# Kernel tuning notes

Hardware: AMD Instinct MI355X
Metric: run time of the kernel (lower is better)

## Reference

```python
import jax, jax.numpy as jnp
import numpy as np

MAX_EMBED = 1024
MAX_HEADS = 16
MIN_WIDTH_RATIO = 0.25


def setup_inputs() -> dict:
    key = jax.random.key(0)
    ks = jax.random.split(key, 10)
    B, S, E = 4, 1024, MAX_EMBED
    query = jax.random.normal(ks[0], (B, S, E), dtype=jnp.float32)
    attention_mask = jax.random.randint(ks[1], (B, 1, 1, S), 0, 2, dtype=jnp.int32)
    # SlimmableLinear params (max sizes); kaiming-ish scale ~ 1/sqrt(fan_in)
    scale = 1.0 / np.sqrt(E)
    def lin(kw, kb):
        w = jax.random.uniform(kw, (E, E), dtype=jnp.float32, minval=-scale, maxval=scale)
        b = jax.random.uniform(kb, (E,), dtype=jnp.float32, minval=-scale, maxval=scale)
        return w, b
    q_w, q_b = lin(ks[2], ks[3])
    k_w, k_b = lin(ks[4], ks[5])
    v_w, v_b = lin(ks[6], ks[7])
    o_w, o_b = lin(ks[8], ks[9])
    return {"query": query, "attention_mask": attention_mask,
            "q_w": q_w, "q_b": q_b, "k_w": k_w, "k_b": k_b,
            "v_w": v_w, "v_b": v_b, "o_w": o_w, "o_b": o_b,
            "width": 768}


def _slim_linear(x, w, b, width):
    # weight stored [out, in] like torch; slice to [width, width]
    return x[..., :width] @ w[:width, :width].T + b[:width]


def reference(query, attention_mask, q_w, q_b, k_w, k_b, v_w, v_b, o_w, o_b, width):
    min_width = int(MAX_EMBED * MIN_WIDTH_RATIO)
    width = max(min_width, min(int(width), MAX_EMBED))
    num_heads = max(1, width * MAX_HEADS // MAX_EMBED)
    head_dim = width // num_heads
    B, S, _ = query.shape

    q = _slim_linear(query, q_w, q_b, width)  # [B,S,width]
    k = _slim_linear(query, k_w, k_b, width)  # key=query (self-attn)
    v = _slim_linear(query, v_w, v_b, width)

    q = q.reshape(B, S, num_heads, head_dim).transpose(0, 2, 1, 3)  # [B,H,S,D]
    k = k.reshape(B, S, num_heads, head_dim).transpose(0, 2, 1, 3)
    v = v.reshape(B, S, num_heads, head_dim).transpose(0, 2, 1, 3)

    scores = jnp.einsum('bhqd,bhkd->bhqk', q, k) / jnp.sqrt(jnp.float32(head_dim))
    scores = jnp.where(attention_mask == 0, jnp.float32(-1e9), scores)
    attn_weights = jax.nn.softmax(scores, axis=-1)  # [B,H,S,S]
    attn_output = jnp.einsum('bhqk,bhkd->bhqd', attn_weights, v)
    attn_output = attn_output.transpose(0, 2, 1, 3).reshape(B, S, width)
    output = attn_output @ o_w[:width, :width].T + o_b[:width]
    return output, attn_weights
```

## Files before the change

### kernel.cpp

```cpp
#include <hip/hip_runtime.h>

#define Bn 4
#define Sn 1024
#define En 1024
#define Wn 768
#define Hn 12
#define Dn 64
#define XE ((size_t)Bn * Sn * Wn)

typedef __attribute__((ext_vector_type(8))) short short8;
typedef __attribute__((ext_vector_type(4))) short short4v;
typedef __attribute__((ext_vector_type(4))) float floatx4;

#define MFMA16(A, B, C) __builtin_amdgcn_mfma_f32_16x16x32_bf16(A, B, C, 0, 0, 0)

__device__ __forceinline__ unsigned short f2bf_rn(float f) {
    unsigned int u = __float_as_uint(f);
    unsigned int r = u + 0x7fffu + ((u >> 16) & 1u);
    return (unsigned short)(r >> 16);
}
__device__ __forceinline__ float bf2f(unsigned short h) {
    return __uint_as_float(((unsigned int)h) << 16);
}

__device__ __forceinline__ void gload_lds16(const unsigned short* g, unsigned short* l) {
    __builtin_amdgcn_global_load_lds(
        (const __attribute__((address_space(1))) void*)g,
        (__attribute__((address_space(3))) void*)l, 16, 0, 0);
}

__global__ __launch_bounds__(256) void prep_kernel(
    const float* __restrict__ x,
    const float* __restrict__ qw, const float* __restrict__ kw,
    const float* __restrict__ vw, const float* __restrict__ ow,
    const float* __restrict__ qb, const float* __restrict__ kb,
    const float* __restrict__ vb,
    unsigned short* __restrict__ xh, unsigned short* __restrict__ xl,
    unsigned short* __restrict__ wqh, unsigned short* __restrict__ wql,
    unsigned short* __restrict__ woh, unsigned short* __restrict__ wol,
    float* __restrict__ bq)
{
    const int bx = blockIdx.x;
    const float* src; unsigned short *dh, *dl; int e;
    if (bx < 3072) {
        e = (bx * 256 + threadIdx.x) * 4;
        src = x; dh = xh; dl = xl;
    } else if (bx < 3072 + 1728) {
        int bb = bx - 3072; int which = bb / 576;
        e = ((bb - which * 576) * 256 + threadIdx.x) * 4;
        src = (which == 0) ? qw : (which == 1) ? kw : vw;
        dh = wqh + (size_t)which * Wn * Wn;
        dl = wql + (size_t)which * Wn * Wn;
    } else if (bx < 3072 + 1728 + 576) {
        e = ((bx - 3072 - 1728) * 256 + threadIdx.x) * 4;
        src = ow; dh = woh; dl = wol;
    } else {
        int t = (bx - 3072 - 1728 - 576) * 256 + threadIdx.x;
        if (t < Wn) bq[t] = qb[t];
        else if (t < 2 * Wn) bq[t] = kb[t - Wn];
        else if (t < 3 * Wn) bq[t] = vb[t - 2 * Wn];
        return;
    }
    int row = e / Wn, col = e - row * Wn;
    float4 v = *(const float4*)(src + (size_t)row * En + col);
    float f[4] = {v.x, v.y, v.z, v.w};
    short4v h, l;
    #pragma unroll
    for (int i = 0; i < 4; ++i) {
        unsigned short hh = f2bf_rn(f[i]);
        h[i] = (short)hh;
        l[i] = (short)f2bf_rn(f[i] - bf2f(hh));
    }
    *(short4v*)(dh + e) = h;
    *(short4v*)(dl + e) = l;
}

__global__ __launch_bounds__(256) void qkv_mfma_kernel(
    const unsigned short* __restrict__ xh, const unsigned short* __restrict__ xl,
    const unsigned short* __restrict__ wh, const unsigned short* __restrict__ wl,
    const float* __restrict__ bq,
    float* __restrict__ q32, float* __restrict__ k32,
    unsigned short* __restrict__ vt_o)
{
    __shared__ __align__(16) unsigned short Ah[128 * 32];
    __shared__ __align__(16) unsigned short Al[128 * 32];
    __shared__ __align__(16) unsigned short Bh[128 * 32];
    __shared__ __align__(16) unsigned short Bl[128 * 32];

    const int tid = threadIdx.x;
    const int wave = tid >> 6, lane = tid & 63;
    const int quad = lane >> 4, l16 = lane & 15;
    const int m0 = blockIdx.x * 128, n0 = blockIdx.y * 128;
    const int wm = wave >> 1, wn = wave & 1;

    floatx4 acc[4][4] = {};

    const unsigned short* gsrc = (wave == 0) ? xh : (wave == 1) ? xl
                               : (wave == 2) ? wh : wl;
    unsigned short* ldst = (wave == 0) ? Ah : (wave == 1) ? Al
                         : (wave == 2) ? Bh : Bl;
    const int base_row = (wave < 2) ? m0 : n0;
    const int r_in = lane >> 2;
    const int cs = (lane & 3) ^ (r_in & 3);

    for (int k0 = 0; k0 < Wn; k0 += 32) {
        #pragma unroll
        for (int i = 0; i < 8; ++i) {
            int r = i * 16 + r_in;
            const unsigned short* gp =
                gsrc + (size_t)(base_row + r) * Wn + k0 + cs * 8;
            gload_lds16(gp, ldst + i * 512);
        }
        __syncthreads();

        short8 afh[4], afl[4], bfh[4], bfl[4];
        #pragma unroll
        for (int t = 0; t < 4; ++t) {
            int mr = wm * 64 + t * 16 + l16;
            int ca = quad ^ (mr & 3);
            afh[t] = *(const short8*)(Ah + mr * 32 + ca * 8);
            afl[t] = *(const short8*)(Al + mr * 32 + ca * 8);
            int nr = wn * 64 + t * 16 + l16;
            int cb = quad ^ (nr & 3);
            bfh[t] = *(const short8*)(Bh + nr * 32 + cb * 8);
            bfl[t] = *(const short8*)(Bl + nr * 32 + cb * 8);
        }
        #pragma unroll
        for (int mt = 0; mt < 4; ++mt)
            #pragma unroll
            for (int nt = 0; nt < 4; ++nt) {
                acc[mt][nt] = MFMA16(afh[mt], bfh[nt], acc[mt][nt]);
                acc[mt][nt] = MFMA16(afh[mt], bfl[nt], acc[mt][nt]);
                acc[mt][nt] = MFMA16(afl[mt], bfh[nt], acc[mt][nt]);
            }
        __syncthreads();
    }

    const int which = n0 / Wn;
    const int b = m0 >> 10;
    #pragma unroll
    for (int nt = 0; nt < 4; ++nt) {
        const int ng = n0 + wn * 64 + nt * 16 + l16;
        const float bias = bq[ng];
        const int f = ng - which * Wn;
        const int h = f >> 6, d = f & 63;
        #pragma unroll
        for (int mt = 0; mt < 4; ++mt) {
            const int mbase = m0 + wm * 64 + mt * 16 + quad * 4;
            const int s0 = mbase & (Sn - 1);
            if (which < 2) {
                float* o32 = which ? k32 : q32;
                size_t idx = (((size_t)(b * Hn + h)) * Sn + s0) * Dn + d;
                #pragma unroll
                for (int r = 0; r < 4; ++r)
                    o32[idx + (size_t)r * Dn] = acc[mt][nt][r] + bias;
            } else {
                size_t idx = (((size_t)(b * Hn + h)) * Dn + d) * Sn + s0;
                short4v pk;
                #pragma unroll
                for (int r = 0; r < 4; ++r)
                    pk[r] = (short)f2bf_rn(acc[mt][nt][r] + bias);
                *(short4v*)(vt_o + idx) = pk;
            }
        }
    }
}

__global__ __launch_bounds__(256) void attn_sum_kernel(
    const float* __restrict__ q32, const float* __restrict__ k32,
    const int* __restrict__ mask, float* __restrict__ lpart)
{
    __shared__ __align__(16) unsigned short Kh[64 * 72];
    __shared__ __align__(16) unsigned short Kl[64 * 72];
    __shared__ float msk[64];

    const int tid = threadIdx.x;
    const int wave = tid >> 6, lane = tid & 63;
    const int quad = lane >> 4, l16 = lane & 15;
    const int qt = blockIdx.x >> 2, ks = blockIdx.x & 3;
    const int h = blockIdx.y, b = blockIdx.z;
    const int bh = b * Hn + h;
    const size_t kvb = (size_t)bh * Sn * Dn;

    short8 qfh[2], qfl[2];
    {
        const int s = qt * 64 + wave * 16 + l16;
        const float* qp = q32 + kvb + (size_t)s * Dn + quad * 8;
        #pragma unroll
        for (int ksp = 0; ksp < 2; ++ksp) {
            float f[8];
            *(float4*)&f[0] = *(const float4*)(qp + ksp * 32);
            *(float4*)&f[4] = *(const float4*)(qp + ksp * 32 + 4);
            #pragma unroll
            for (int j = 0; j < 8; ++j) {
                unsigned short hh = f2bf_rn(f[j]);
                qfh[ksp][j] = (short)hh;
                qfl[ksp][j] = (short)f2bf_rn(f[j] - bf2f(hh));
            }
        }
    }

    const int sr = tid >> 2, sc = tid & 3;
    float lsum[4] = {0.f, 0.f, 0.f, 0.f};

    for (int kt = 0; kt < 4; ++kt) {
        __syncthreads();
        {
            const float* kp = k32 + kvb + (size_t)(ks * 256 + kt * 64 + sr) * Dn + sc * 16;
            float f[16];
            *(float4*)&f[0]  = *(const float4*)(kp);
            *(float4*)&f[4]  = *(const float4*)(kp + 4);
            *(float4*)&f[8]  = *(const float4*)(kp + 8);
            *(float4*)&f[12] = *(const float4*)(kp + 12);
            short8 h0, h1, l0, l1;
            #pragma unroll
            for (int j = 0; j < 8; ++j) {
                unsigned short hh = f2bf_rn(f[j]);
                h0[j] = (short)hh; l0[j] = (short)f2bf_rn(f[j] - bf2f(hh));
                unsigned short hh2 = f2bf_rn(f[8 + j]);
                h1[j] = (short)hh2; l1[j] = (short)f2bf_rn(f[8 + j] - bf2f(hh2));
            }
            *(short8*)&Kh[sr * 72 + sc * 16]     = h0;
            *(short8*)&Kh[sr * 72 + sc * 16 + 8] = h1;
            *(short8*)&Kl[sr * 72 + sc * 16]     = l0;
            *(short8*)&Kl[sr * 72 + sc * 16 + 8] = l1;
            if (tid < 64) msk[tid] = (float)mask[b * Sn + ks * 256 + kt * 64 + tid];
        }
        __syncthreads();
        #pragma unroll
        for (int ct = 0; ct < 4; ++ct) {
            floatx4 acc = {0.f, 0.f, 0.f, 0.f};
            const int key = ct * 16 + l16;
            #pragma unroll
            for (int ksp = 0; ksp < 2; ++ksp) {
                short8 b8h = *(const short8*)&Kh[key * 72 + ksp * 32 + quad * 8];
                short8 b8l = *(const short8*)&Kl[key * 72 + ksp * 32 + quad * 8];
                acc = MFMA16(qfh[ksp], b8h, acc);
                acc = MFMA16(qfh[ksp], b8l, acc);
                acc = MFMA16(qfl[ksp], b8h, acc);
            }
            const float mv = msk[key];
            #pragma unroll
            for (int r = 0; r < 4; ++r)
                lsum[r] += __expf(acc[r] * 0.125f) * mv;
        }
    }

    #pragma unroll
    for (int r = 0; r < 4; ++r) {
        float v = lsum[r];
        v += __shfl_xor(v, 1, 64);
        v += __shfl_xor(v, 2, 64);
        v += __shfl_xor(v, 4, 64);
        v += __shfl_xor(v, 8, 64);
        lsum[r] = v;
    }
    if (l16 == 0) {
        const int row = qt * 64 + wave * 16 + quad * 4;
        #pragma unroll
        for (int r = 0; r < 4; ++r)
            lpart[((size_t)ks * Bn * Hn + bh) * Sn + row + r] = lsum[r];
    }
}

__global__ __launch_bounds__(256) void attn_out_kernel(
    const float* __restrict__ q32, const float* __restrict__ k32,
    const unsigned short* __restrict__ vt, const int* __restrict__ mask,
    const float* __restrict__ lpart, float* __restrict__ attn,
    float* __restrict__ opart)
{
    __shared__ __align__(16) unsigned short Kh[64 * 72];
    __shared__ __align__(16) unsigned short Kl[64 * 72];
    __shared__ __align__(16) unsigned short Vs[64 * 72];
    __shared__ __align__(16) unsigned short Ps[4][16 * 72];
    __shared__ float msk[64];

    const int tid = threadIdx.x;
    const int wave = tid >> 6, lane = tid & 63;
    const int quad = lane >> 4, l16 = lane & 15;
    const int qt = blockIdx.x >> 2, ks = blockIdx.x & 3;
    const int h = blockIdx.y, b = blockIdx.z;
    const int bh = b * Hn + h;
    const size_t kvb = (size_t)bh * Sn * Dn;

    short8 qfh[2], qfl[2];
    {
        const int s = qt * 64 + wave * 16 + l16;
        const float* qp = q32 + kvb + (size_t)s * Dn + quad * 8;
        #pragma unroll
        for (int ksp = 0; ksp < 2; ++ksp) {
            float f[8];
            *(float4*)&f[0] = *(const float4*)(qp + ksp * 32);
            *(float4*)&f[4] = *(const float4*)(qp + ksp * 32 + 4);
            #pragma unroll
            for (int j = 0; j < 8; ++j) {
                unsigned short hh = f2bf_rn(f[j]);
                qfh[ksp][j] = (short)hh;
                qfl[ksp][j] = (short)f2bf_rn(f[j] - bf2f(hh));
            }
        }
    }

    float li[4];
    {
        const int row = qt * 64 + wave * 16 + quad * 4;
        #pragma unroll
        for (int r = 0; r < 4; ++r) {
            float lv = 0.f;
            #pragma unroll
            for (int s4 = 0; s4 < 4; ++s4)
                lv += lpart[((size_t)s4 * Bn * Hn + bh) * Sn + row + r];
            li[r] = (lv > 0.f) ? 1.f / lv : 0.f;
        }
    }

    const int sr = tid >> 2, sc = tid & 3;
    const size_t vbase = (size_t)bh * Dn * Sn;
    floatx4 oacc[4] = {};

    for (int kt = 0; kt < 4; ++kt) {
        __syncthreads();
        {
            const float* kp = k32 + kvb + (size_t)(ks * 256 + kt * 64 + sr) * Dn + sc * 16;
            float f[16];
            *(float4*)&f[0]  = *(const float4*)(kp);
            *(float4*)&f[4]  = *(const float4*)(kp + 4);
            *(float4*)&f[8]  = *(const float4*)(kp + 8);
            *(float4*)&f[12] = *(const float4*)(kp + 12);
            short8 h0, h1, l0, l1;
            #pragma unroll
            for (int j = 0; j < 8; ++j) {
                unsigned short hh = f2bf_rn(f[j]);
                h0[j] = (short)hh; l0[j] = (short)f2bf_rn(f[j] - bf2f(hh));
                unsigned short hh2 = f2bf_rn(f[8 + j]);
                h1[j] = (short)hh2; l1[j] = (short)f2bf_rn(f[8 + j] - bf2f(hh2));
            }
            *(short8*)&Kh[sr * 72 + sc * 16]     = h0;
            *(short8*)&Kh[sr * 72 + sc * 16 + 8] = h1;
            *(short8*)&Kl[sr * 72 + sc * 16]     = l0;
            *(short8*)&Kl[sr * 72 + sc * 16 + 8] = l1;
            const size_t g2 = vbase + (size_t)sr * Sn + ks * 256 + kt * 64 + sc * 16;
            *(short8*)&Vs[sr * 72 + sc * 16]     = *(const short8*)(vt + g2);
            *(short8*)&Vs[sr * 72 + sc * 16 + 8] = *(const short8*)(vt + g2 + 8);
            if (tid < 64) msk[tid] = (float)mask[b * Sn + ks * 256 + kt * 64 + tid];
        }
        __syncthreads();

        #pragma unroll
        for (int ct = 0; ct < 4; ++ct) {
            floatx4 acc = {0.f, 0.f, 0.f, 0.f};
            const int key = ct * 16 + l16;
            #pragma unroll
            for (int ksp = 0; ksp < 2; ++ksp) {
                short8 b8h = *(const short8*)&Kh[key * 72 + ksp * 32 + quad * 8];
                short8 b8l = *(const short8*)&Kl[key * 72 + ksp * 32 + quad * 8];
                acc = MFMA16(qfh[ksp], b8h, acc);
                acc = MFMA16(qfh[ksp], b8l, acc);
                acc = MFMA16(qfl[ksp], b8h, acc);
            }
            const float mv = msk[key];
            const int row0 = qt * 64 + wave * 16 + quad * 4;
            const int key_g = ks * 256 + kt * 64 + key;
            #pragma unroll
            for (int r = 0; r < 4; ++r) {
                float p = __expf(acc[r] * 0.125f) * mv * li[r];
                attn[((size_t)bh * Sn + row0 + r) * Sn + key_g] = p;
                Ps[wave][(quad * 4 + r) * 72 + key] = f2bf_rn(p);
            }
        }
        #pragma unroll
        for (int ksp = 0; ksp < 2; ++ksp) {
            short8 pf = *(const short8*)&Ps[wave][l16 * 72 + ksp * 32 + quad * 8];
            #pragma unroll
            for (int dt = 0; dt < 4; ++dt) {
                short8 vf = *(const short8*)&Vs[(dt * 16 + l16) * 72 + ksp * 32 + quad * 8];
                oacc[dt] = MFMA16(pf, vf, oacc[dt]);
            }
        }
    }

    const int s0 = qt * 64 + wave * 16 + quad * 4;
    #pragma unroll
    for (int dt = 0; dt < 4; ++dt)
        #pragma unroll
        for (int r = 0; r < 4; ++r)
            opart[(size_t)ks * XE + ((size_t)b * Sn + s0 + r) * Wn
                  + h * Dn + dt * 16 + l16] = oacc[dt][r];
}

__global__ __launch_bounds__(256) void reduce_ao_kernel(
    const float* __restrict__ opart, unsigned short* __restrict__ aoh,
    unsigned short* __restrict__ aol)
{
    size_t e = ((size_t)blockIdx.x * 256 + threadIdx.x) * 4;
    float4 a0 = *(const float4*)(opart + e);
    float4 a1 = *(const float4*)(opart + XE + e);
    float4 a2 = *(const float4*)(opart + 2 * XE + e);
    float4 a3 = *(const float4*)(opart + 3 * XE + e);
    float f[4] = {a0.x + a1.x + a2.x + a3.x, a0.y + a1.y + a2.y + a3.y,
                  a0.z + a1.z + a2.z + a3.z, a0.w + a1.w + a2.w + a3.w};
    short4v h, l;
    #pragma unroll
    for (int i = 0; i < 4; ++i) {
        unsigned short hh = f2bf_rn(f[i]);
        h[i] = (short)hh;
        l[i] = (short)f2bf_rn(f[i] - bf2f(hh));
    }
    *(short4v*)(aoh + e) = h;
    *(short4v*)(aol + e) = l;
}

__global__ __launch_bounds__(256) void oproj_mfma_kernel(
    const unsigned short* __restrict__ aoh, const unsigned short* __restrict__ aol,
    const unsigned short* __restrict__ wh, const unsigned short* __restrict__ wl,
    const float* __restrict__ ob, float* __restrict__ out)
{
    __shared__ __align__(16) unsigned short Ah[64 * 32];
    __shared__ __align__(16) unsigned short Al[64 * 32];
    __shared__ __align__(16) unsigned short Bh[128 * 32];
    __shared__ __align__(16) unsigned short Bl[128 * 32];

    const int tid = threadIdx.x;
    const int wave = tid >> 6, lane = tid & 63;
    const int quad = lane >> 4, l16 = lane & 15;
    const int m0 = blockIdx.x * 64, n0 = blockIdx.y * 128;
    const int wm = wave >> 1, wn = wave & 1;

    floatx4 acc[2][4] = {};

    const int r_in = lane >> 2;
    const int cs = (lane & 3) ^ (r_in & 3);

    for (int k0 = 0; k0 < Wn; k0 += 32) {
        if (wave == 0) {
            #pragma unroll
            for (int i = 0; i < 4; ++i) {
                gload_lds16(aoh + (size_t)(m0 + i * 16 + r_in) * Wn + k0 + cs * 8,
                            Ah + i * 512);
                gload_lds16(aol + (size_t)(m0 + i * 16 + r_in) * Wn + k0 + cs * 8,
                            Al + i * 512);
            }
        } else if (wave == 1) {
            #pragma unroll
            for (int i = 0; i < 8; ++i)
                gload_lds16(wh + (size_t)(n0 + i * 16 + r_in) * Wn + k0 + cs * 8,
                            Bh + i * 512);
        } else if (wave == 2) {
            #pragma unroll
            for (int i = 0; i < 8; ++i)
                gload_lds16(wl + (size_t)(n0 + i * 16 + r_in) * Wn + k0 + cs * 8,
                            Bl + i * 512);
        }
        __syncthreads();

        short8 afh[2], afl[2], bfh[4], bfl[4];
        #pragma unroll
        for (int t = 0; t < 2; ++t) {
            int mr = wm * 32 + t * 16 + l16;
            int ca = quad ^ (mr & 3);
            afh[t] = *(const short8*)(Ah + mr * 32 + ca * 8);
            afl[t] = *(const short8*)(Al + mr * 32 + ca * 8);
        }
        #pragma unroll
        for (int t = 0; t < 4; ++t) {
            int nr = wn * 64 + t * 16 + l16;
            int cb = quad ^ (nr & 3);
            bfh[t] = *(const short8*)(Bh + nr * 32 + cb * 8);
            bfl[t] = *(const short8*)(Bl + nr * 32 + cb * 8);
        }
        #pragma unroll
        for (int mt = 0; mt < 2; ++mt)
            #pragma unroll
            for (int nt = 0; nt < 4; ++nt) {
                acc[mt][nt] = MFMA16(afh[mt], bfh[nt], acc[mt][nt]);
                acc[mt][nt] = MFMA16(afh[mt], bfl[nt], acc[mt][nt]);
                acc[mt][nt] = MFMA16(afl[mt], bfh[nt], acc[mt][nt]);
            }
        __syncthreads();
    }

    #pragma unroll
    for (int nt = 0; nt < 4; ++nt) {
        const int ng = n0 + wn * 64 + nt * 16 + l16;
        const float bias = ob[ng];
        #pragma unroll
        for (int mt = 0; mt < 2; ++mt) {
            const int m = m0 + wm * 32 + mt * 16 + quad * 4;
            #pragma unroll
            for (int r = 0; r < 4; ++r)
                out[(size_t)(m + r) * Wn + ng] = acc[mt][nt][r] + bias;
        }
    }
}

extern "C" void kernel_launch(void* const* d_in, const int* in_sizes, int n_in,
                              void* d_out, int out_size, void* d_ws, size_t ws_size,
                              hipStream_t stream) {
    const float* x    = (const float*)d_in[0];
    const int*   mask = (const int*)  d_in[1];
    const float* qw = (const float*)d_in[2];
    const float* qb = (const float*)d_in[3];
    const float* kw = (const float*)d_in[4];
    const float* kb = (const float*)d_in[5];
    const float* vw = (const float*)d_in[6];
    const float* vb = (const float*)d_in[7];
    const float* ow = (const float*)d_in[8];
    const float* ob = (const float*)d_in[9];

    float* out  = (float*)d_out;
    float* attn = out + XE;

    char* w = (char*)d_ws;
    unsigned short* xh   = (unsigned short*)w;  w += XE * 2;
    unsigned short* xl   = (unsigned short*)w;  w += XE * 2;
    unsigned short* wqh  = (unsigned short*)w;  w += (size_t)3 * Wn * Wn * 2;
    unsigned short* wql  = (unsigned short*)w;  w += (size_t)3 * Wn * Wn * 2;
    unsigned short* woh  = (unsigned short*)w;  w += (size_t)Wn * Wn * 2;
    unsigned short* wol  = (unsigned short*)w;  w += (size_t)Wn * Wn * 2;
    float*          bq   = (float*)w;           w += (size_t)3 * Wn * 4;
    float*          q32  = (float*)w;           w += XE * 4;
    float*          k32  = (float*)w;           w += XE * 4;
    unsigned short* vt_w = (unsigned short*)w;  w += XE * 2;
    float*          lpart = (float*)w;          w += (size_t)4 * Bn * Hn * Sn * 4;
    float*          opart = (float*)w;          w += (size_t)4 * XE * 4;

    prep_kernel<<<5385, 256, 0, stream>>>(x, qw, kw, vw, ow, qb, kb, vb,
                                          xh, xl, wqh, wql, woh, wol, bq);

    qkv_mfma_kernel<<<dim3(32, 18), 256, 0, stream>>>(
        xh, xl, wqh, wql, bq, q32, k32, vt_w);

    attn_sum_kernel<<<dim3(64, Hn, Bn), 256, 0, stream>>>(
        q32, k32, mask, lpart);

    attn_out_kernel<<<dim3(64, Hn, Bn), 256, 0, stream>>>(
        q32, k32, vt_w, mask, lpart, attn, opart);

    reduce_ao_kernel<<<3072, 256, 0, stream>>>(opart, xh, xl);

    oproj_mfma_kernel<<<dim3(64, 6), 256, 0, stream>>>(
        xh, xl, woh, wol, ob, out);
}
```

Baseline: 443.6 us.

## Use single bf16 Q/K, read K/V directly, and fuse the split-key reduction into attn_out

The QKV projection now stores Q and K as single bf16 values, and drops the low-part A term for those outputs. Both attention kernels then run one MFMA pass per score instead of three split-precision passes, and read K and V fragments straight from global memory instead of staging them in LDS. attn_out now walks all keys per block, so the 4-way key-split partial outputs and the separate reduce kernel go away, and it writes the hi/lo bf16 attention output directly. This cuts conversion work, MFMA count, syncs and partial-buffer traffic. The cost is lower precision in the scores and attention weights, which may break accuracy tolerances, plus fewer blocks and uncached global fragment loads in attn_out.

```diff
diff --git a/kernel.cpp b/kernel.cpp
--- a/kernel.cpp
+++ b/kernel.cpp
@@ -79,7 +79,7 @@
     const unsigned short* __restrict__ xh, const unsigned short* __restrict__ xl,
     const unsigned short* __restrict__ wh, const unsigned short* __restrict__ wl,
     const float* __restrict__ bq,
-    float* __restrict__ q32, float* __restrict__ k32,
+    unsigned short* __restrict__ qh_o, unsigned short* __restrict__ kh_o,
     unsigned short* __restrict__ vt_o)
 {
     __shared__ __align__(16) unsigned short Ah[128 * 32];
@@ -92,6 +92,8 @@
     const int quad = lane >> 4, l16 = lane & 15;
     const int m0 = blockIdx.x * 128, n0 = blockIdx.y * 128;
     const int wm = wave >> 1, wn = wave & 1;
+    const int which = n0 / Wn;
+    const bool full = (which == 2);
 
     floatx4 acc[4][4] = {};
 
@@ -104,12 +106,14 @@
     const int cs = (lane & 3) ^ (r_in & 3);
 
     for (int k0 = 0; k0 < Wn; k0 += 32) {
-        #pragma unroll
-        for (int i = 0; i < 8; ++i) {
-            int r = i * 16 + r_in;
-            const unsigned short* gp =
-                gsrc + (size_t)(base_row + r) * Wn + k0 + cs * 8;
-            gload_lds16(gp, ldst + i * 512);
+        if (full || wave != 1) {
+            #pragma unroll
+            for (int i = 0; i < 8; ++i) {
+                int r = i * 16 + r_in;
+                const unsigned short* gp =
+                    gsrc + (size_t)(base_row + r) * Wn + k0 + cs * 8;
+                gload_lds16(gp, ldst + i * 512);
+            }
         }
         __syncthreads();
 
@@ -119,7 +123,7 @@
             int mr = wm * 64 + t * 16 + l16;
             int ca = quad ^ (mr & 3);
             afh[t] = *(const short8*)(Ah + mr * 32 + ca * 8);
-            afl[t] = *(const short8*)(Al + mr * 32 + ca * 8);
+            if (full) afl[t] = *(const short8*)(Al + mr * 32 + ca * 8);
             int nr = wn * 64 + t * 16 + l16;
             int cb = quad ^ (nr & 3);
             bfh[t] = *(const short8*)(Bh + nr * 32 + cb * 8);
@@ -131,12 +135,11 @@
             for (int nt = 0; nt < 4; ++nt) {
                 acc[mt][nt] = MFMA16(afh[mt], bfh[nt], acc[mt][nt]);
                 acc[mt][nt] = MFMA16(afh[mt], bfl[nt], acc[mt][nt]);
-                acc[mt][nt] = MFMA16(afl[mt], bfh[nt], acc[mt][nt]);
+                if (full) acc[mt][nt] = MFMA16(afl[mt], bfh[nt], acc[mt][nt]);
             }
         __syncthreads();
     }
 
-    const int which = n0 / Wn;
     const int b = m0 >> 10;
     #pragma unroll
     for (int nt = 0; nt < 4; ++nt) {
@@ -149,11 +152,11 @@
             const int mbase = m0 + wm * 64 + mt * 16 + quad * 4;
             const int s0 = mbase & (Sn - 1);
             if (which < 2) {
-                float* o32 = which ? k32 : q32;
+                unsigned short* oq = which ? kh_o : qh_o;
                 size_t idx = (((size_t)(b * Hn + h)) * Sn + s0) * Dn + d;
                 #pragma unroll
                 for (int r = 0; r < 4; ++r)
-                    o32[idx + (size_t)r * Dn] = acc[mt][nt][r] + bias;
+                    oq[idx + (size_t)r * Dn] = f2bf_rn(acc[mt][nt][r] + bias);
             } else {
                 size_t idx = (((size_t)(b * Hn + h)) * Dn + d) * Sn + s0;
                 short4v pk;
@@ -167,13 +170,9 @@
 }
 
 __global__ __launch_bounds__(256) void attn_sum_kernel(
-    const float* __restrict__ q32, const float* __restrict__ k32,
+    const unsigned short* __restrict__ qh, const unsigned short* __restrict__ kh,
     const int* __restrict__ mask, float* __restrict__ lpart)
 {
-    __shared__ __align__(16) unsigned short Kh[64 * 72];
-    __shared__ __align__(16) unsigned short Kl[64 * 72];
-    __shared__ float msk[64];
-
     const int tid = threadIdx.x;
     const int wave = tid >> 6, lane = tid & 63;
     const int quad = lane >> 4, l16 = lane & 15;
@@ -182,64 +181,27 @@
     const int bh = b * Hn + h;
     const size_t kvb = (size_t)bh * Sn * Dn;
 
-    short8 qfh[2], qfl[2];
+    short8 qf[2];
     {
         const int s = qt * 64 + wave * 16 + l16;
-        const float* qp = q32 + kvb + (size_t)s * Dn + quad * 8;
-        #pragma unroll
-        for (int ksp = 0; ksp < 2; ++ksp) {
-            float f[8];
-            *(float4*)&f[0] = *(const float4*)(qp + ksp * 32);
-            *(float4*)&f[4] = *(const float4*)(qp + ksp * 32 + 4);
-            #pragma unroll
-            for (int j = 0; j < 8; ++j) {
-                unsigned short hh = f2bf_rn(f[j]);
-                qfh[ksp][j] = (short)hh;
-                qfl[ksp][j] = (short)f2bf_rn(f[j] - bf2f(hh));
-            }
-        }
-    }
-
-    const int sr = tid >> 2, sc = tid & 3;
+        const unsigned short* qp = qh + kvb + (size_t)s * Dn + quad * 8;
+        qf[0] = *(const short8*)(qp);
+        qf[1] = *(const short8*)(qp + 32);
+    }
+
     float lsum[4] = {0.f, 0.f, 0.f, 0.f};
 
     for (int kt = 0; kt < 4; ++kt) {
-        __syncthreads();
-        {
-            const float* kp = k32 + kvb + (size_t)(ks * 256 + kt * 64 + sr) * Dn + sc * 16;
-            float f[16];
-            *(float4*)&f[0]  = *(const float4*)(kp);
-            *(float4*)&f[4]  = *(const float4*)(kp + 4);
-            *(float4*)&f[8]  = *(const float4*)(kp + 8);
-            *(float4*)&f[12] = *(const float4*)(kp + 12);
-            short8 h0, h1, l0, l1;
-            #pragma unroll
-            for (int j = 0; j < 8; ++j) {
-                unsigned short hh = f2bf_rn(f[j]);
-                h0[j] = (short)hh; l0[j] = (short)f2bf_rn(f[j] - bf2f(hh));
-                unsigned short hh2 = f2bf_rn(f[8 + j]);
-                h1[j] = (short)hh2; l1[j] = (short)f2bf_rn(f[8 + j] - bf2f(hh2));
-            }
-            *(short8*)&Kh[sr * 72 + sc * 16]     = h0;
-            *(short8*)&Kh[sr * 72 + sc * 16 + 8] = h1;
-            *(short8*)&Kl[sr * 72 + sc * 16]     = l0;
-            *(short8*)&Kl[sr * 72 + sc * 16 + 8] = l1;
-            if (tid < 64) msk[tid] = (float)mask[b * Sn + ks * 256 + kt * 64 + tid];
-        }
-        __syncthreads();
         #pragma unroll
         for (int ct = 0; ct < 4; ++ct) {
+            const int key = ks * 256 + kt * 64 + ct * 16 + l16;
+            const unsigned short* kp = kh + kvb + (size_t)key * Dn + quad * 8;
+            short8 kf0 = *(const short8*)(kp);
+            short8 kf1 = *(const short8*)(kp + 32);
             floatx4 acc = {0.f, 0.f, 0.f, 0.f};
-            const int key = ct * 16 + l16;
-            #pragma unroll
-            for (int ksp = 0; ksp < 2; ++ksp) {
-                short8 b8h = *(const short8*)&Kh[key * 72 + ksp * 32 + quad * 8];
-                short8 b8l = *(const short8*)&Kl[key * 72 + ksp * 32 + quad * 8];
-                acc = MFMA16(qfh[ksp], b8h, acc);
-                acc = MFMA16(qfh[ksp], b8l, acc);
-                acc = MFMA16(qfl[ksp], b8h, acc);
-            }
-            const float mv = msk[key];
+            acc = MFMA16(qf[0], kf0, acc);
+            acc = MFMA16(qf[1], kf1, acc);
+            const float mv = (float)mask[b * Sn + key];
             #pragma unroll
             for (int r = 0; r < 4; ++r)
                 lsum[r] += __expf(acc[r] * 0.125f) * mv;
@@ -264,108 +226,60 @@
 }
 
 __global__ __launch_bounds__(256) void attn_out_kernel(
-    const float* __restrict__ q32, const float* __restrict__ k32,
+    const unsigned short* __restrict__ qh, const unsigned short* __restrict__ kh,
     const unsigned short* __restrict__ vt, const int* __restrict__ mask,
     const float* __restrict__ lpart, float* __restrict__ attn,
-    float* __restrict__ opart)
+    unsigned short* __restrict__ aoh, unsigned short* __restrict__ aol)
 {
-    __shared__ __align__(16) unsigned short Kh[64 * 72];
-    __shared__ __align__(16) unsigned short Kl[64 * 72];
-    __shared__ __align__(16) unsigned short Vs[64 * 72];
     __shared__ __align__(16) unsigned short Ps[4][16 * 72];
-    __shared__ float msk[64];
 
     const int tid = threadIdx.x;
     const int wave = tid >> 6, lane = tid & 63;
     const int quad = lane >> 4, l16 = lane & 15;
-    const int qt = blockIdx.x >> 2, ks = blockIdx.x & 3;
+    const int qt = blockIdx.x;
     const int h = blockIdx.y, b = blockIdx.z;
     const int bh = b * Hn + h;
     const size_t kvb = (size_t)bh * Sn * Dn;
-
-    short8 qfh[2], qfl[2];
+    const size_t vbase = (size_t)bh * Dn * Sn;
+
+    short8 qf[2];
     {
         const int s = qt * 64 + wave * 16 + l16;
-        const float* qp = q32 + kvb + (size_t)s * Dn + quad * 8;
-        #pragma unroll
-        for (int ksp = 0; ksp < 2; ++ksp) {
-            float f[8];
-            *(float4*)&f[0] = *(const float4*)(qp + ksp * 32);
-            *(float4*)&f[4] = *(const float4*)(qp + ksp * 32 + 4);
-            #pragma unroll
-            for (int j = 0; j < 8; ++j) {
-                unsigned short hh = f2bf_rn(f[j]);
-                qfh[ksp][j] = (short)hh;
-                qfl[ksp][j] = (short)f2bf_rn(f[j] - bf2f(hh));
-            }
-        }
-    }
-
+        const unsigned short* qp = qh + kvb + (size_t)s * Dn + quad * 8;
+        qf[0] = *(const short8*)(qp);
+        qf[1] = *(const short8*)(qp + 32);
+    }
+
+    const int row0 = qt * 64 + wave * 16 + quad * 4;
     float li[4];
-    {
-        const int row = qt * 64 + wave * 16 + quad * 4;
-        #pragma unroll
-        for (int r = 0; r < 4; ++r) {
-            float lv = 0.f;
-            #pragma unroll
-            for (int s4 = 0; s4 < 4; ++s4)
-                lv += lpart[((size_t)s4 * Bn * Hn + bh) * Sn + row + r];
-            li[r] = (lv > 0.f) ? 1.f / lv : 0.f;
-        }
-    }
-
-    const int sr = tid >> 2, sc = tid & 3;
-    const size_t vbase = (size_t)bh * Dn * Sn;
+    #pragma unroll
+    for (int r = 0; r < 4; ++r) {
+        float lv = 0.f;
+        #pragma unroll
+        for (int s4 = 0; s4 < 4; ++s4)
+            lv += lpart[((size_t)s4 * Bn * Hn + bh) * Sn + row0 + r];
+        li[r] = (lv > 0.f) ? 1.f / lv : 0.f;
+    }
+
     floatx4 oacc[4] = {};
 
-    for (int kt = 0; kt < 4; ++kt) {
-        __syncthreads();
-        {
-            const float* kp = k32 + kvb + (size_t)(ks * 256 + kt * 64 + sr) * Dn + sc * 16;
-            float f[16];
-            *(float4*)&f[0]  = *(const float4*)(kp);
-            *(float4*)&f[4]  = *(const float4*)(kp + 4);
-            *(float4*)&f[8]  = *(const float4*)(kp + 8);
-            *(float4*)&f[12] = *(const float4*)(kp + 12);
-            short8 h0, h1, l0, l1;
-            #pragma unroll
-            for (int j = 0; j < 8; ++j) {
-                unsigned short hh = f2bf_rn(f[j]);
-                h0[j] = (short)hh; l0[j] = (short)f2bf_rn(f[j] - bf2f(hh));
-                unsigned short hh2 = f2bf_rn(f[8 + j]);
-                h1[j] = (short)hh2; l1[j] = (short)f2bf_rn(f[8 + j] - bf2f(hh2));
-            }
-            *(short8*)&Kh[sr * 72 + sc * 16]     = h0;
-            *(short8*)&Kh[sr * 72 + sc * 16 + 8] = h1;
-            *(short8*)&Kl[sr * 72 + sc * 16]     = l0;
-            *(short8*)&Kl[sr * 72 + sc * 16 + 8] = l1;
-            const size_t g2 = vbase + (size_t)sr * Sn + ks * 256 + kt * 64 + sc * 16;
-            *(short8*)&Vs[sr * 72 + sc * 16]     = *(const short8*)(vt + g2);
-            *(short8*)&Vs[sr * 72 + sc * 16 + 8] = *(const short8*)(vt + g2 + 8);
-            if (tid < 64) msk[tid] = (float)mask[b * Sn + ks * 256 + kt * 64 + tid];
-        }
-        __syncthreads();
-
+    for (int kk = 0; kk < 16; ++kk) {
+        const int k0 = kk * 64;
         #pragma unroll
         for (int ct = 0; ct < 4; ++ct) {
+            const int key = k0 + ct * 16 + l16;
+            const unsigned short* kp = kh + kvb + (size_t)key * Dn + quad * 8;
+            short8 kf0 = *(const short8*)(kp);
+            short8 kf1 = *(const short8*)(kp + 32);
             floatx4 acc = {0.f, 0.f, 0.f, 0.f};
-            const int key = ct * 16 + l16;
-            #pragma unroll
-            for (int ksp = 0; ksp < 2; ++ksp) {
-                short8 b8h = *(const short8*)&Kh[key * 72 + ksp * 32 + quad * 8];
-                short8 b8l = *(const short8*)&Kl[key * 72 + ksp * 32 + quad * 8];
-                acc = MFMA16(qfh[ksp], b8h, acc);
-                acc = MFMA16(qfh[ksp], b8l, acc);
-                acc = MFMA16(qfl[ksp], b8h, acc);
-            }
-            const float mv = msk[key];
-            const int row0 = qt * 64 + wave * 16 + quad * 4;
-            const int key_g = ks * 256 + kt * 64 + key;
+            acc = MFMA16(qf[0], kf0, acc);
+            acc = MFMA16(qf[1], kf1, acc);
+            const float mv = (float)mask[b * Sn + key];
             #pragma unroll
             for (int r = 0; r < 4; ++r) {
-                float p = __expf(acc[r] * 0.125f) * mv * li[r];
-                attn[((size_t)bh * Sn + row0 + r) * Sn + key_g] = p;
-                Ps[wave][(quad * 4 + r) * 72 + key] = f2bf_rn(p);
+                const float p = __expf(acc[r] * 0.125f) * mv * li[r];
+                attn[((size_t)bh * Sn + row0 + r) * Sn + key] = p;
+                Ps[wave][(quad * 4 + r) * 72 + ct * 16 + l16] = f2bf_rn(p);
             }
         }
         #pragma unroll
@@ -373,41 +287,24 @@
             short8 pf = *(const short8*)&Ps[wave][l16 * 72 + ksp * 32 + quad * 8];
             #pragma unroll
             for (int dt = 0; dt < 4; ++dt) {
-                short8 vf = *(const short8*)&Vs[(dt * 16 + l16) * 72 + ksp * 32 + quad * 8];
+                short8 vf = *(const short8*)(vt + vbase
+                              + (size_t)(dt * 16 + l16) * Sn + k0 + ksp * 32 + quad * 8);
                 oacc[dt] = MFMA16(pf, vf, oacc[dt]);
             }
         }
     }
 
-    const int s0 = qt * 64 + wave * 16 + quad * 4;
-    #pragma unroll
-    for (int dt = 0; dt < 4; ++dt)
-        #pragma unroll
-        for (int r = 0; r < 4; ++r)
-            opart[(size_t)ks * XE + ((size_t)b * Sn + s0 + r) * Wn
-                  + h * Dn + dt * 16 + l16] = oacc[dt][r];
-}
-
-__global__ __launch_bounds__(256) void reduce_ao_kernel(
-    const float* __restrict__ opart, unsigned short* __restrict__ aoh,
-    unsigned short* __restrict__ aol)
-{
-    size_t e = ((size_t)blockIdx.x * 256 + threadIdx.x) * 4;
-    float4 a0 = *(const float4*)(opart + e);
-    float4 a1 = *(const float4*)(opart + XE + e);
-    float4 a2 = *(const float4*)(opart + 2 * XE + e);
-    float4 a3 = *(const float4*)(opart + 3 * XE + e);
-    float f[4] = {a0.x + a1.x + a2.x + a3.x, a0.y + a1.y + a2.y + a3.y,
-                  a0.z + a1.z + a2.z + a3.z, a0.w + a1.w + a2.w + a3.w};
-    short4v h, l;
-    #pragma unroll
-    for (int i = 0; i < 4; ++i) {
-        unsigned short hh = f2bf_rn(f[i]);
-        h[i] = (short)hh;
-        l[i] = (short)f2bf_rn(f[i] - bf2f(hh));
-    }
-    *(short4v*)(aoh + e) = h;
-    *(short4v*)(aol + e) = l;
+    #pragma unroll
+    for (int dt = 0; dt < 4; ++dt) {
+        #pragma unroll
+        for (int r = 0; r < 4; ++r) {
+            const float o = oacc[dt][r];
+            const unsigned short hh = f2bf_rn(o);
+            const size_t idx = ((size_t)b * Sn + row0 + r) * Wn + h * Dn + dt * 16 + l16;
+            aoh[idx] = hh;
+            aol[idx] = f2bf_rn(o - bf2f(hh));
+        }
+    }
 }
 
 __global__ __launch_bounds__(256) void oproj_mfma_kernel(
@@ -518,25 +415,22 @@
     unsigned short* woh  = (unsigned short*)w;  w += (size_t)Wn * Wn * 2;
     unsigned short* wol  = (unsigned short*)w;  w += (size_t)Wn * Wn * 2;
     float*          bq   = (float*)w;           w += (size_t)3 * Wn * 4;
-    float*          q32  = (float*)w;           w += XE * 4;
-    float*          k32  = (float*)w;           w += XE * 4;
+    unsigned short* qh   = (unsigned short*)w;  w += XE * 2;
+    unsigned short* kh   = (unsigned short*)w;  w += XE * 2;
     unsigned short* vt_w = (unsigned short*)w;  w += XE * 2;
     float*          lpart = (float*)w;          w += (size_t)4 * Bn * Hn * Sn * 4;
-    float*          opart = (float*)w;          w += (size_t)4 * XE * 4;
 
     prep_kernel<<<5385, 256, 0, stream>>>(x, qw, kw, vw, ow, qb, kb, vb,
                                           xh, xl, wqh, wql, woh, wol, bq);
 
     qkv_mfma_kernel<<<dim3(32, 18), 256, 0, stream>>>(
-        xh, xl, wqh, wql, bq, q32, k32, vt_w);
+        xh, xl, wqh, wql, bq, qh, kh, vt_w);
 
     attn_sum_kernel<<<dim3(64, Hn, Bn), 256, 0, stream>>>(
-        q32, k32, mask, lpart);
-
-    attn_out_kernel<<<dim3(64, Hn, Bn), 256, 0, stream>>>(
-        q32, k32, vt_w, mask, lpart, attn, opart);
-
-    reduce_ao_kernel<<<3072, 256, 0, stream>>>(opart, xh, xl);
+        qh, kh, mask, lpart);
+
+    attn_out_kernel<<<dim3(16, Hn, Bn), 256, 0, stream>>>(
+        qh, kh, vt_w, mask, lpart, attn, xh, xl);
 
     oproj_mfma_kernel<<<dim3(64, 6), 256, 0, stream>>>(
         xh, xl, woh, wol, ob, out);
```

New measurement: 462.5 us. 4.2% more time.
